# Kernel optimization log

Hardware: AMD Instinct MI355X
Metric: run time of the kernel (lower is better)

The kernel has to match this reference:

```python
import jax, jax.numpy as jnp
import numpy as np

DIM = 256
NUM_HEADS = 4
HEAD_DIM = DIM // NUM_HEADS


def _linear_params(k, d_in, d_out):
    kw, kb = jax.random.split(k)
    lim = 1.0 / np.sqrt(d_in)
    W = jax.random.uniform(kw, (d_out, d_in), jnp.float32, -lim, lim)
    b = jax.random.uniform(kb, (d_out,), jnp.float32, -lim, lim)
    return W, b


def setup_inputs() -> dict:
    key = jax.random.key(0)
    ks = jax.random.split(key, 10)
    B, Nq, Nkv = 8, 4096, 256
    inp = {
        'node_emb': jax.random.normal(ks[0], (B, Nq, DIM), jnp.float32),
        'cluster_emb': jax.random.normal(ks[1], (B, Nkv, DIM), jnp.float32),
        'clustering_weights': jax.random.normal(ks[2], (B, Nq, Nkv), jnp.float32),
        'ln_q_g': jnp.ones((DIM,), jnp.float32), 'ln_q_b': jnp.zeros((DIM,), jnp.float32),
        'ln_kv_g': jnp.ones((DIM,), jnp.float32), 'ln_kv_b': jnp.zeros((DIM,), jnp.float32),
        'ln_out_g': jnp.ones((DIM,), jnp.float32), 'ln_out_b': jnp.zeros((DIM,), jnp.float32),
    }
    for name, k in [('q', ks[3]), ('k', ks[4]), ('v', ks[5]), ('o', ks[6])]:
        W, b = _linear_params(k, DIM, DIM)
        inp[f'W_{name}'], inp[f'b_{name}'] = W, b
    W1, b1 = _linear_params(ks[7], DIM, DIM)
    W2, b2 = _linear_params(ks[8], DIM, DIM)
    inp.update(W_m1=W1, b_m1=b1, W_m2=W2, b_m2=b2)
    return inp


def _layer_norm(x, g, b, eps=1e-5):
    mu = jnp.mean(x, axis=-1, keepdims=True)
    var = jnp.var(x, axis=-1, keepdims=True)
    return (x - mu) * jax.lax.rsqrt(var + eps) * g + b


def reference(node_emb, cluster_emb, clustering_weights,
              ln_q_g, ln_q_b, ln_kv_g, ln_kv_b, ln_out_g, ln_out_b,
              W_q, b_q, W_k, b_k, W_v, b_v, W_o, b_o,
              W_m1, b_m1, W_m2, b_m2):
    B, Nq, D = node_emb.shape
    Nkv = cluster_emb.shape[1]
    q_in = _layer_norm(node_emb, ln_q_g, ln_q_b)
    kv_in = _layer_norm(cluster_emb, ln_kv_g, ln_kv_b)
    # projections -> [B, H, N, hd]
    Q = (q_in @ W_q.T + b_q).reshape(B, Nq, NUM_HEADS, HEAD_DIM).transpose(0, 2, 1, 3)
    K = (kv_in @ W_k.T + b_k).reshape(B, Nkv, NUM_HEADS, HEAD_DIM).transpose(0, 2, 1, 3)
    V = (kv_in @ W_v.T + b_v).reshape(B, Nkv, NUM_HEADS, HEAD_DIM).transpose(0, 2, 1, 3)
    scores = jnp.einsum('bhqd,bhkd->bhqk', Q, K) / np.sqrt(HEAD_DIM)
    scores = scores + clustering_weights[:, None, :, :]
    attn = jax.nn.softmax(scores, axis=-1)
    ctx = jnp.einsum('bhqk,bhkd->bhqd', attn, V)
    ctx = ctx.transpose(0, 2, 1, 3).reshape(B, Nq, D)
    attn_out = ctx @ W_o.T + b_o
    x = node_emb + attn_out
    h = _layer_norm(x, ln_out_g, ln_out_b)
    h = jax.nn.gelu(h @ W_m1.T + b_m1, approximate=False) @ W_m2.T + b_m2
    out = x + h
    attn_matrix = attn.mean(axis=1)
    return out, attn_matrix
```

## Files before the change

kernel.cpp:

```cpp
#include <hip/hip_runtime.h>
#include <math.h>

typedef __attribute__((ext_vector_type(8))) short short8;
typedef __attribute__((ext_vector_type(4))) float f32x4;
typedef __attribute__((ext_vector_type(2))) unsigned int u32x2;

#define AS1 __attribute__((address_space(1)))
#define AS3 __attribute__((address_space(3)))

__device__ __forceinline__ float b2f(short s){
  return __uint_as_float(((unsigned int)(unsigned short)s) << 16);
}
__device__ __forceinline__ short f2b(float f){
  unsigned int u = __float_as_uint(f);
  u = (u + 0x7fffu + ((u >> 16) & 1u)) >> 16;
  return (short)u;
}
__device__ __forceinline__ unsigned pk2(float lo, float hi){
  return ((unsigned)(unsigned short)f2b(hi) << 16) | (unsigned)(unsigned short)f2b(lo);
}
__device__ __forceinline__ float ulo(unsigned u){ return __uint_as_float(u << 16); }
__device__ __forceinline__ float uhi(unsigned u){ return __uint_as_float(u & 0xffff0000u); }

__global__ __launch_bounds__(256) void cvt_w(
    const float* __restrict__ s0, const float* __restrict__ s1,
    const float* __restrict__ s2, const float* __restrict__ s3,
    const float* __restrict__ s4, const float* __restrict__ s5,
    short* __restrict__ dst, short* __restrict__ dstS)
{
  const float* srcs[6] = {s0, s1, s2, s3, s4, s5};
  int i = blockIdx.x * 256 + threadIdx.x;
  int mat = i >> 16, rc = i & 65535;
  short v = f2b(srcs[mat][rc]);
  dst[i] = v;
  int slot = (mat >= 3) ? (mat - 3) : (mat == 0 ? 3 : -1);
  if (slot >= 0){
    int row = rc >> 8, col = rc & 255;
    int d2 = slot * 65536 + ((col >> 5) << 13) + (row << 5)
           + (((col >> 3) & 3) << 3) + (col & 7);
    dstS[d2] = v;
  }
}

__global__ __launch_bounds__(256, 2) void kv_k(
    const float* __restrict__ cluster,
    const short* __restrict__ Wk, const short* __restrict__ Wv,
    const float* __restrict__ b_k, const float* __restrict__ b_v,
    const float* __restrict__ lng, const float* __restrict__ lnb,
    short* __restrict__ kfrag, short* __restrict__ vfrag)
{
  __shared__ short As[64][264];
  __shared__ short Ws[2][256][40];
  const int tid = threadIdx.x;
  const int m0 = blockIdx.x << 6;
  const int w = tid >> 6, lane = tid & 63;
  const int l15 = lane & 15, g = lane >> 4;

  {
    const int row = tid >> 2, c0 = (tid & 3) << 6;
    float vv[64];
    const float* src = &cluster[(size_t)(m0 + row) * 256 + c0];
    #pragma unroll
    for (int i = 0; i < 16; ++i) *(f32x4*)&vv[4 * i] = *(const f32x4*)&src[4 * i];
    float s1 = 0.f, s2 = 0.f;
    #pragma unroll
    for (int i = 0; i < 64; ++i){ s1 += vv[i]; s2 += vv[i] * vv[i]; }
    s1 += __shfl_xor(s1, 1); s2 += __shfl_xor(s2, 1);
    s1 += __shfl_xor(s1, 2); s2 += __shfl_xor(s2, 2);
    const float mu = s1 * 0.00390625f;
    const float rs = rsqrtf(s2 * 0.00390625f - mu * mu + 1e-5f);
    #pragma unroll
    for (int i = 0; i < 8; ++i){
      f32x4 gv0 = *(const f32x4*)&lng[c0 + 8 * i];
      f32x4 gv1 = *(const f32x4*)&lng[c0 + 8 * i + 4];
      f32x4 bv0 = *(const f32x4*)&lnb[c0 + 8 * i];
      f32x4 bv1 = *(const f32x4*)&lnb[c0 + 8 * i + 4];
      short8 o;
      #pragma unroll
      for (int j = 0; j < 4; ++j) o[j] = f2b((vv[8 * i + j] - mu) * rs * gv0[j] + bv0[j]);
      #pragma unroll
      for (int j = 0; j < 4; ++j) o[4 + j] = f2b((vv[8 * i + 4 + j] - mu) * rs * gv1[j] + bv1[j]);
      *(short8*)&As[row][c0 + 8 * i] = o;
    }
  }

  f32x4 acc[16];
  const int row_l = (w << 4) + (g << 2);

#define KV_LOOP(WMAT)                                                                 \
  do{                                                                                 \
    _Pragma("unroll")                                                                 \
    for (int it = 0; it < 4; ++it){                                                   \
      int row = (it << 6) + (tid >> 2), c = (tid & 3) << 3;                           \
      *(short8*)&Ws[0][row][c] = *(const short8*)&(WMAT)[(size_t)row * 256 + c];      \
    }                                                                                 \
    __syncthreads();                                                                  \
    _Pragma("unroll")                                                                 \
    for (int nt = 0; nt < 16; ++nt) acc[nt] = (f32x4){0.f, 0.f, 0.f, 0.f};            \
    int cur = 0;                                                                      \
    for (int s = 0; s < 8; ++s){                                                      \
      const int k0 = s << 5;                                                          \
      short8 wreg[4];                                                                 \
      if (s < 7){                                                                     \
        _Pragma("unroll")                                                             \
        for (int it = 0; it < 4; ++it)                                                \
          wreg[it] = *(const short8*)&(WMAT)[(size_t)((it << 6) + (tid >> 2)) * 256 + k0 + 32 + ((tid & 3) << 3)]; \
      }                                                                               \
      short8 af = *(const short8*)&As[(w << 4) + l15][k0 + (g << 3)];                 \
      _Pragma("unroll")                                                               \
      for (int nt = 0; nt < 16; ++nt){                                                \
        short8 bf = *(const short8*)&Ws[cur][(nt << 4) + l15][g << 3];                \
        acc[nt] = __builtin_amdgcn_mfma_f32_16x16x32_bf16(af, bf, acc[nt], 0, 0, 0);  \
      }                                                                               \
      if (s < 7){                                                                     \
        _Pragma("unroll")                                                             \
        for (int it = 0; it < 4; ++it)                                                \
          *(short8*)&Ws[cur ^ 1][(it << 6) + (tid >> 2)][(tid & 3) << 3] = wreg[it];  \
      }                                                                               \
      __syncthreads();                                                                \
      cur ^= 1;                                                                       \
    }                                                                                 \
  }while(0)

  KV_LOOP(Wk);
  #pragma unroll
  for (int nt = 0; nt < 16; ++nt){
    const int col = (nt << 4) + l15;
    const float bv = b_k[col];
    #pragma unroll
    for (int r = 0; r < 4; ++r){
      const int m = m0 + row_l + r;
      float v = acc[nt][r] + bv;
      const int b_ = m >> 8, kvr = m & 255;
      const int knt = kvr >> 4, kl = kvr & 15;
      const int h = col >> 6, half = (col >> 5) & 1, kg = (col >> 3) & 3, kj = col & 7;
      kfrag[(((((size_t)(b_ * 4 + h) * 16 + knt) * 2 + half) * 4 + kg) * 16 + kl) * 8 + kj] = f2b(v);
    }
  }
  KV_LOOP(Wv);
  #pragma unroll
  for (int nt = 0; nt < 16; ++nt){
    const int col = (nt << 4) + l15;
    const float bv = b_v[col];
    #pragma unroll
    for (int r = 0; r < 4; ++r){
      const int m = m0 + row_l + r;
      float v = acc[nt][r] + bv;
      const int b_ = m >> 8, kvj = m & 255;
      const int jp = (kvj & ~31) | (((kvj >> 2) & 3) << 3) | (((kvj >> 4) & 1) << 2) | (kvj & 3);
      const int h = col >> 6, dp = col & 63;
      const int kk = jp >> 5, vg = (jp >> 3) & 3, vj = jp & 7;
      const int vn2 = dp >> 4, vl = dp & 15;
      vfrag[(((((size_t)(b_ * 4 + h) * 8 + kk) * 4 + vn2) * 4 + vg) * 16 + vl) * 8 + vj] = f2b(v);
    }
  }
#undef KV_LOOP
}

__global__ __launch_bounds__(512, 4) void qgemm_k(
    const float* __restrict__ node, const short* __restrict__ Wq,
    const float* __restrict__ bias,
    const float* __restrict__ lng, const float* __restrict__ lnb,
    short* __restrict__ outB)
{
  extern __shared__ __align__(16) short lds[];
  short* Ws0 = lds + 16896;
  short* Ws1 = Ws0 + 8192;
  const int tid = threadIdx.x;
  const int tile = blockIdx.x;
  const int m0 = tile << 6;
  const int w = tid >> 6, lane = tid & 63;
  const int l15 = lane & 15, g = lane >> 4;
  const int wm = w >> 1, wn = w & 1;
  const int row_l = (wm << 4) + (g << 2);
  const int colb = wn << 7;

#define ASW8(row_, col0_) (*(short8*)((char*)lds + (row_) * 528 + \
    (((col0_) << 1) ^ ((((row_) >> 2) & 3) << 4))))
#define ASR8(row_, boff_) (*(const short8*)((char*)lds + (row_) * 528 + \
    ((boff_) ^ ((((row_) >> 2) & 3) << 4))))
#define STGW(dst_, wmat_, s_) do{ _Pragma("unroll")                                  \
  for (int it_ = 0; it_ < 2; ++it_){ int c_ = (it_ << 9) + tid;                      \
    __builtin_amdgcn_global_load_lds(                                               \
        (const AS1 void*)((wmat_) + ((size_t)(s_) << 13) + (c_ << 3)),              \
        (AS3 void*)((dst_) + (c_ << 3)), 16, 0, 0); } }while(0)

  {
    const int row = tid >> 3, c0 = (tid & 7) << 5;
    float vv[32];
    const float* src = &node[(size_t)(m0 + row) * 256 + c0];
    #pragma unroll
    for (int i = 0; i < 8; ++i) *(f32x4*)&vv[4 * i] = *(const f32x4*)&src[4 * i];
    float s1 = 0.f, s2 = 0.f;
    #pragma unroll
    for (int i = 0; i < 32; ++i){ s1 += vv[i]; s2 += vv[i] * vv[i]; }
    s1 += __shfl_xor(s1, 1); s2 += __shfl_xor(s2, 1);
    s1 += __shfl_xor(s1, 2); s2 += __shfl_xor(s2, 2);
    s1 += __shfl_xor(s1, 4); s2 += __shfl_xor(s2, 4);
    const float mu = s1 * 0.00390625f;
    const float rs = rsqrtf(s2 * 0.00390625f - mu * mu + 1e-5f);
    #pragma unroll
    for (int i = 0; i < 4; ++i){
      const int col0 = c0 + 8 * i;
      f32x4 g0 = *(const f32x4*)&lng[col0], g1 = *(const f32x4*)&lng[col0 + 4];
      f32x4 b0 = *(const f32x4*)&lnb[col0], b1 = *(const f32x4*)&lnb[col0 + 4];
      short8 o;
      #pragma unroll
      for (int j = 0; j < 4; ++j) o[j] = f2b((vv[8 * i + j] - mu) * rs * g0[j] + b0[j]);
      #pragma unroll
      for (int j = 0; j < 4; ++j) o[4 + j] = f2b((vv[8 * i + 4 + j] - mu) * rs * g1[j] + b1[j]);
      ASW8(row, col0) = o;
    }
  }
  STGW(Ws0, Wq, 0);
  __syncthreads();

  f32x4 acc[8];
  #pragma unroll
  for (int ntl = 0; ntl < 8; ++ntl) acc[ntl] = {0.f, 0.f, 0.f, 0.f};
  {
    int cur = 0;
    #pragma unroll
    for (int s = 0; s < 8; ++s){
      short* rbuf = cur ? Ws1 : Ws0;
      short* sbuf = cur ? Ws0 : Ws1;
      if (s < 7){ STGW(sbuf, Wq, s + 1);
        asm volatile("s_waitcnt vmcnt(2)" ::: "memory");
      } else {
        asm volatile("s_waitcnt vmcnt(0)" ::: "memory");
      }
      __builtin_amdgcn_s_barrier();
      __builtin_amdgcn_sched_barrier(0);
      const short8 af = ASR8((wm << 4) + l15, (s << 6) + (g << 4));
      __builtin_amdgcn_s_setprio(1);
      #pragma unroll
      for (int ntl = 0; ntl < 8; ++ntl){
        short8 bf = *(const short8*)&rbuf[(((wn << 3) + ntl) * 16 + l15) * 32 + (g << 3)];
        acc[ntl] = __builtin_amdgcn_mfma_f32_16x16x32_bf16(af, bf, acc[ntl], 0, 0, 0);
      }
      __builtin_amdgcn_s_setprio(0);
      __builtin_amdgcn_s_barrier();
      __builtin_amdgcn_sched_barrier(0);
      cur ^= 1;
    }
  }
  #pragma unroll
  for (int ntl = 0; ntl < 8; ++ntl){
    const int col = colb + (ntl << 4) + l15;
    const float bv = bias[col];
    #pragma unroll
    for (int r = 0; r < 4; ++r){
      float v = acc[ntl][r] + bv;
      outB[((((size_t)tile * 8 + (col >> 5)) * 4 + wm) * 64
            + (((col >> 3) & 3) << 4) + (g << 2) + r) * 8 + (col & 7)] = f2b(v);
    }
  }
#undef ASW8
#undef ASR8
#undef STGW
}

__global__ __launch_bounds__(256, 2) void attn_k(
    const short* __restrict__ Qf, const short* __restrict__ Kf,
    const short* __restrict__ Vf, const float* __restrict__ cw,
    short* __restrict__ ctx, float* __restrict__ am_out)
{
  extern __shared__ __align__(16) short smem[];
  short* Kl = smem;
  short* Vl = smem + 16384;
  const int b = blockIdx.y;
  const int q0 = blockIdx.x << 6;
  const int tid = threadIdx.x;
  const int w = tid >> 6, lane = tid & 63;
  const int l15 = lane & 15, g = lane >> 4;
  const size_t qw = (size_t)b * 4096 + q0 + (w << 4);
  const size_t qblk = qw >> 4;
  const size_t tileQ = qblk >> 2;
  const int wQ = (int)(qblk & 3);
  const size_t tileC = (size_t)b * 64 + blockIdx.x;

#define STG(dst_, src_) do{ _Pragma("unroll")                                        \
  for (int it_ = 0; it_ < 8; ++it_){ int c_ = (it_ << 8) + tid;                      \
    __builtin_amdgcn_global_load_lds((const AS1 void*)((src_) + (c_ << 3)),          \
                                     (AS3 void*)((dst_) + (c_ << 3)), 16, 0, 0); } }while(0)

  STG(Kl, Kf + ((size_t)(b * 4) << 14));

  unsigned cwp[16][2];
  f32x4 am[16];
  {
    char* reg = (char*)smem + 32768 + (w << 13);
    #pragma unroll
    for (int j = 0; j < 16; ++j){
      f32x4 v = *(const f32x4*)&cw[(qw + j) * 256 + (lane << 2)];
      u32x2 d = { pk2(v[0], v[1]), pk2(v[2], v[3]) };
      unsigned off = ((j << 9) + (lane << 3)) ^ ((j & 7) << 4);
      *(u32x2*)(reg + off) = d;
    }
    __syncthreads();
    #pragma unroll
    for (int nt = 0; nt < 16; ++nt){
      unsigned base = ((l15 << 9) + (nt << 5) + (g << 3)) ^ ((l15 & 7) << 4);
      cwp[nt][0] = *(const unsigned*)(reg + base);
      cwp[nt][1] = *(const unsigned*)(reg + base + 4);
      am[nt] = {0.f, 0.f, 0.f, 0.f};
    }
    __syncthreads();
  }

  for (int h = 0; h < 4; ++h){
    STG(Vl, Vf + ((size_t)(b * 4 + h) << 14));
    short8 qf0 = *(const short8*)&Qf[(((tileQ * 8 + (h << 1)) * 4 + wQ) * 64 + lane) * 8];
    short8 qf1 = *(const short8*)&Qf[(((tileQ * 8 + (h << 1) + 1) * 4 + wQ) * 64 + lane) * 8];

    f32x4 acc[16];
    #pragma unroll
    for (int nt = 0; nt < 16; ++nt) acc[nt] = {0.f, 0.f, 0.f, 0.f};
    __builtin_amdgcn_s_setprio(1);
    #pragma unroll
    for (int nt = 0; nt < 16; ++nt){
      short8 kf0 = *(const short8*)&Kl[(nt << 10) + (lane << 3)];
      acc[nt] = __builtin_amdgcn_mfma_f32_16x16x32_bf16(kf0, qf0, acc[nt], 0, 0, 0);
      short8 kf1 = *(const short8*)&Kl[(nt << 10) + 512 + (lane << 3)];
      acc[nt] = __builtin_amdgcn_mfma_f32_16x16x32_bf16(kf1, qf1, acc[nt], 0, 0, 0);
    }
    __builtin_amdgcn_s_setprio(0);
    __syncthreads();
    if (h < 3) STG(Kl, Kf + ((size_t)(b * 4 + h + 1) << 14));

    float mx = -3.4e38f;
    #pragma unroll
    for (int nt = 0; nt < 16; ++nt){
      float c0 = __uint_as_float(cwp[nt][0] << 16);
      float c1 = __uint_as_float(cwp[nt][0] & 0xffff0000u);
      float c2 = __uint_as_float(cwp[nt][1] << 16);
      float c3 = __uint_as_float(cwp[nt][1] & 0xffff0000u);
      acc[nt][0] = acc[nt][0] * 0.125f + c0;
      acc[nt][1] = acc[nt][1] * 0.125f + c1;
      acc[nt][2] = acc[nt][2] * 0.125f + c2;
      acc[nt][3] = acc[nt][3] * 0.125f + c3;
      mx = fmaxf(mx, fmaxf(fmaxf(acc[nt][0], acc[nt][1]), fmaxf(acc[nt][2], acc[nt][3])));
    }
    mx = fmaxf(mx, __shfl_xor(mx, 16));
    mx = fmaxf(mx, __shfl_xor(mx, 32));
    float sm = 0.f;
    #pragma unroll
    for (int nt = 0; nt < 16; ++nt){
      #pragma unroll
      for (int r = 0; r < 4; ++r){
        float e = __expf(acc[nt][r] - mx);
        acc[nt][r] = e; sm += e;
      }
    }
    sm += __shfl_xor(sm, 16);
    sm += __shfl_xor(sm, 32);
    float inv = 1.f / sm;
    #pragma unroll
    for (int nt = 0; nt < 16; ++nt){
      #pragma unroll
      for (int r = 0; r < 4; ++r){
        float p = acc[nt][r] * inv;
        acc[nt][r] = p;
        am[nt][r] += 0.25f * p;
      }
    }
    f32x4 oc[4] = {{0,0,0,0},{0,0,0,0},{0,0,0,0},{0,0,0,0}};
    __builtin_amdgcn_s_setprio(1);
    #pragma unroll
    for (int kk = 0; kk < 8; ++kk){
      union { short8 s; unsigned u[4]; } pa;
      pa.u[0] = pk2(acc[2 * kk][0],     acc[2 * kk][1]);
      pa.u[1] = pk2(acc[2 * kk][2],     acc[2 * kk][3]);
      pa.u[2] = pk2(acc[2 * kk + 1][0], acc[2 * kk + 1][1]);
      pa.u[3] = pk2(acc[2 * kk + 1][2], acc[2 * kk + 1][3]);
      #pragma unroll
      for (int n2 = 0; n2 < 4; ++n2){
        short8 vb = *(const short8*)&Vl[(((kk << 2) + n2) << 9) + (lane << 3)];
        oc[n2] = __builtin_amdgcn_mfma_f32_16x16x32_bf16(pa.s, vb, oc[n2], 0, 0, 0);
      }
    }
    __builtin_amdgcn_s_setprio(0);
    #pragma unroll
    for (int n2 = 0; n2 < 4; ++n2){
      const int sctx = (h << 1) + (n2 >> 1);
      const int gctx = ((n2 & 1) << 1) + (l15 >> 3);
      const int j = l15 & 7;
      #pragma unroll
      for (int r = 0; r < 4; ++r)
        ctx[(((tileC * 8 + sctx) * 4 + w) * 64 + (gctx << 4) + (g << 2) + r) * 8 + j]
            = f2b(oc[n2][r]);
    }
    __syncthreads();
  }

  {
    char* reg = (char*)smem + (w << 14);
    #pragma unroll
    for (int nt = 0; nt < 16; ++nt){
      unsigned off = ((l15 << 10) + (nt << 6) + (g << 4)) ^ ((l15 & 7) << 4);
      *(f32x4*)(reg + off) = am[nt];
    }
    __syncthreads();
    #pragma unroll
    for (int i2 = 0; i2 < 16; ++i2){
      unsigned fb = (tid << 4) + (i2 << 12);
      unsigned rowin = (fb >> 10) & 15;
      f32x4 v = *(const f32x4*)((char*)smem + (fb ^ ((rowin & 7) << 4)));
      unsigned row = fb >> 10;
      *(f32x4*)&am_out[((size_t)b * 4096 + q0 + row) * 256 + ((fb & 1023) >> 2)] = v;
    }
  }
#undef STG
}

__global__ __launch_bounds__(512, 4) void tail_k(
    const short* __restrict__ ctxaf, const short* __restrict__ Wst,
    const float* __restrict__ b_o, const float* __restrict__ b_m1,
    const float* __restrict__ b_m2, const float* __restrict__ node,
    const float* __restrict__ lng, const float* __restrict__ lnb,
    float* __restrict__ outF)
{
  extern __shared__ __align__(16) short lds[];
  short* Ws0 = lds + 16896;
  short* Ws1 = Ws0 + 8192;
  float* part = (float*)(lds + 33280);
  const int tid = threadIdx.x;
  const int tile = blockIdx.x;
  const int m0 = tile << 6;
  const int w = tid >> 6, lane = tid & 63;
  const int l15 = lane & 15, g = lane >> 4;
  const int wm = w >> 1, wn = w & 1;
  const int row_l = (wm << 4) + (g << 2);
  const int colb = wn << 7;

#define ASW(row_, col_) (*(short*)((char*)lds + (row_) * 528 + \
    (((col_) ^ ((((row_) >> 2) & 3) << 3)) << 1)))
#define ASR8(row_, boff_) (*(const short8*)((char*)lds + (row_) * 528 + \
    ((boff_) ^ ((((row_) >> 2) & 3) << 4))))
#define STGW(dst_, wmat_, s_) do{ _Pragma("unroll")                                  \
  for (int it_ = 0; it_ < 2; ++it_){ int c_ = (it_ << 9) + tid;                      \
    __builtin_amdgcn_global_load_lds(                                               \
        (const AS1 void*)((wmat_) + ((size_t)(s_) << 13) + (c_ << 3)),              \
        (AS3 void*)((dst_) + (c_ << 3)), 16, 0, 0); } }while(0)
#define KLOOP(WMAT, AF_EXPR)                                                         \
  do{ int cur = 0;                                                                   \
    _Pragma("unroll")                                                                \
    for (int s = 0; s < 8; ++s){                                                     \
      short* rbuf = cur ? Ws1 : Ws0;                                                 \
      short* sbuf = cur ? Ws0 : Ws1;                                                 \
      if (s < 7){ STGW(sbuf, WMAT, s + 1);                                           \
        asm volatile("s_waitcnt vmcnt(2)" ::: "memory");                             \
      } else {                                                                       \
        asm volatile("s_waitcnt vmcnt(0)" ::: "memory");                             \
      }                                                                              \
      __builtin_amdgcn_s_barrier();                                                  \
      __builtin_amdgcn_sched_barrier(0);                                             \
      const short8 af = (AF_EXPR);                                                   \
      __builtin_amdgcn_s_setprio(1);                                                 \
      _Pragma("unroll")                                                              \
      for (int ntl = 0; ntl < 8; ++ntl){                                             \
        short8 bf = *(const short8*)&rbuf[(((wn << 3) + ntl) * 16 + l15) * 32 + (g << 3)]; \
        acc[ntl] = __builtin_amdgcn_mfma_f32_16x16x32_bf16(af, bf, acc[ntl], 0, 0, 0); \
      }                                                                              \
      __builtin_amdgcn_s_setprio(0);                                                 \
      __builtin_amdgcn_s_barrier();                                                  \
      __builtin_amdgcn_sched_barrier(0);                                             \
      cur ^= 1;                                                                      \
    } }while(0)

  f32x4 acc[8];

  STGW(Ws0, Wst, 0);
  short8 afr[8];
  #pragma unroll
  for (int s = 0; s < 8; ++s)
    afr[s] = *(const short8*)&ctxaf[((((size_t)tile << 3) + s) * 4 + wm) * 512 + (lane << 3)];
  #pragma unroll
  for (int ntl = 0; ntl < 8; ++ntl) acc[ntl] = {0.f, 0.f, 0.f, 0.f};
  KLOOP(Wst, afr[s]);

  unsigned xvp[8][2];
  #pragma unroll
  for (int ntl = 0; ntl < 8; ++ntl){
    const int col = colb + (ntl << 4) + l15;
    const float bv = b_o[col];
    float x0 = acc[ntl][0] + bv + node[(size_t)(m0 + row_l + 0) * 256 + col];
    float x1 = acc[ntl][1] + bv + node[(size_t)(m0 + row_l + 1) * 256 + col];
    float x2 = acc[ntl][2] + bv + node[(size_t)(m0 + row_l + 2) * 256 + col];
    float x3 = acc[ntl][3] + bv + node[(size_t)(m0 + row_l + 3) * 256 + col];
    xvp[ntl][0] = pk2(x0, x1);
    xvp[ntl][1] = pk2(x2, x3);
  }
  #pragma unroll
  for (int r = 0; r < 4; ++r){
    float s1 = 0.f, s2 = 0.f;
    #pragma unroll
    for (int ntl = 0; ntl < 8; ++ntl){
      float v = (r == 0) ? ulo(xvp[ntl][0]) : (r == 1) ? uhi(xvp[ntl][0])
              : (r == 2) ? ulo(xvp[ntl][1]) : uhi(xvp[ntl][1]);
      s1 += v; s2 += v * v;
    }
    #pragma unroll
    for (int off = 1; off < 16; off <<= 1){ s1 += __shfl_xor(s1, off); s2 += __shfl_xor(s2, off); }
    if (l15 == 0){
      part[((row_l + r) * 2 + wn) * 2]     = s1;
      part[((row_l + r) * 2 + wn) * 2 + 1] = s2;
    }
  }
  __syncthreads();
  #pragma unroll
  for (int r = 0; r < 4; ++r){
    const int row = row_l + r;
    const float S1 = part[(row * 2) * 2]     + part[(row * 2 + 1) * 2];
    const float S2 = part[(row * 2) * 2 + 1] + part[(row * 2 + 1) * 2 + 1];
    const float mu = S1 * 0.00390625f;
    const float rs = rsqrtf(S2 * 0.00390625f - mu * mu + 1e-5f);
    #pragma unroll
    for (int ntl = 0; ntl < 8; ++ntl){
      const int col = colb + (ntl << 4) + l15;
      float v = (r == 0) ? ulo(xvp[ntl][0]) : (r == 1) ? uhi(xvp[ntl][0])
              : (r == 2) ? ulo(xvp[ntl][1]) : uhi(xvp[ntl][1]);
      ASW(row, col) = f2b((v - mu) * rs * lng[col] + lnb[col]);
    }
  }

  {
    const short* Wm1 = Wst + 65536;
    STGW(Ws0, Wm1, 0);
    __syncthreads();
    #pragma unroll
    for (int ntl = 0; ntl < 8; ++ntl) acc[ntl] = {0.f, 0.f, 0.f, 0.f};
    KLOOP(Wm1, ASR8((wm << 4) + l15, (s << 6) + (g << 4)));
  }
  #pragma unroll
  for (int ntl = 0; ntl < 8; ++ntl){
    const int col = colb + (ntl << 4) + l15;
    const float bv = b_m1[col];
    #pragma unroll
    for (int r = 0; r < 4; ++r){
      float v = acc[ntl][r] + bv;
      v = 0.5f * v * (1.0f + erff(v * 0.70710678118f));
      ASW(row_l + r, col) = f2b(v);
    }
  }

  {
    const short* Wm2 = Wst + 131072;
    STGW(Ws0, Wm2, 0);
    __syncthreads();
    #pragma unroll
    for (int ntl = 0; ntl < 8; ++ntl) acc[ntl] = {0.f, 0.f, 0.f, 0.f};
    KLOOP(Wm2, ASR8((wm << 4) + l15, (s << 6) + (g << 4)));
  }
  #pragma unroll
  for (int ntl = 0; ntl < 8; ++ntl){
    const int col = colb + (ntl << 4) + l15;
    const float bv = b_m2[col];
    #pragma unroll
    for (int r = 0; r < 4; ++r){
      float xr = (r == 0) ? ulo(xvp[ntl][0]) : (r == 1) ? uhi(xvp[ntl][0])
               : (r == 2) ? ulo(xvp[ntl][1]) : uhi(xvp[ntl][1]);
      outF[(size_t)(m0 + row_l + r) * 256 + col] = acc[ntl][r] + bv + xr;
    }
  }
#undef ASW
#undef ASR8
#undef STGW
#undef KLOOP
}

extern "C" void kernel_launch(void* const* d_in, const int* in_sizes, int n_in,
                              void* d_out, int out_size, void* d_ws, size_t ws_size,
                              hipStream_t stream)
{
  const float* node_emb = (const float*)d_in[0];
  const float* cluster  = (const float*)d_in[1];
  const float* cw       = (const float*)d_in[2];
  const float* ln_q_g   = (const float*)d_in[3];
  const float* ln_q_b   = (const float*)d_in[4];
  const float* ln_kv_g  = (const float*)d_in[5];
  const float* ln_kv_b  = (const float*)d_in[6];
  const float* ln_o_g   = (const float*)d_in[7];
  const float* ln_o_b   = (const float*)d_in[8];
  const float* W_q  = (const float*)d_in[9];  const float* b_q  = (const float*)d_in[10];
  const float* W_k  = (const float*)d_in[11]; const float* b_k  = (const float*)d_in[12];
  const float* W_v  = (const float*)d_in[13]; const float* b_v  = (const float*)d_in[14];
  const float* W_o  = (const float*)d_in[15]; const float* b_o  = (const float*)d_in[16];
  const float* W_m1 = (const float*)d_in[17]; const float* b_m1 = (const float*)d_in[18];
  const float* W_m2 = (const float*)d_in[19]; const float* b_m2 = (const float*)d_in[20];

  char* ws = (char*)d_ws;
  short* Wbf   = (short*)ws;
  short* Wst   = (short*)(ws + 786432);
  short* bufA  = (short*)(ws + 1310720);
  short* bufB  = (short*)(ws + 1310720 + 16777216);
  short* kfrag = (short*)(ws + 1310720 + 2 * 16777216);
  short* vfrag = (short*)(ws + 1310720 + 2 * 16777216 + 1048576);

  float* outF = (float*)d_out;
  float* amof = (float*)d_out + 8388608;

  hipFuncSetAttribute((const void*)attn_k,  hipFuncAttributeMaxDynamicSharedMemorySize, 65536);
  hipFuncSetAttribute((const void*)tail_k,  hipFuncAttributeMaxDynamicSharedMemorySize, 67584);
  hipFuncSetAttribute((const void*)qgemm_k, hipFuncAttributeMaxDynamicSharedMemorySize, 66560);

  cvt_w<<<1536, 256, 0, stream>>>(W_q, W_k, W_v, W_o, W_m1, W_m2, Wbf, Wst);
  kv_k<<<32, 256, 0, stream>>>(cluster, Wbf + 65536, Wbf + 131072,
      b_k, b_v, ln_kv_g, ln_kv_b, kfrag, vfrag);
  qgemm_k<<<512, 512, 66560, stream>>>(node_emb, Wst + 196608, b_q,
      ln_q_g, ln_q_b, bufB);
  attn_k<<<dim3(64, 8), 256, 65536, stream>>>(bufB, kfrag, vfrag, cw, bufA, amof);
  tail_k<<<512, 512, 67584, stream>>>(bufA, Wst, b_o, b_m1, b_m2,
      node_emb, ln_o_g, ln_o_b, outF);
}
```

Baseline: 115.5 us.

## Split attention key dimension across two waves per query block

The attention kernel now runs 512 threads per block, and pairs of waves split the 256 keys for each 16-query group. Row max and row sum are combined through small LDS buffers behind extra barriers, and the partial P·V outputs are added through LDS before the context is written. The goal is to halve per-wave register pressure (accumulators, clustering weights, attention-mean state) and raise the number of resident waves so latency is hidden better. In exchange it adds several block-wide barriers per head and extra LDS traffic for the reductions.

```diff
diff --git a/kernel.cpp b/kernel.cpp
--- a/kernel.cpp
+++ b/kernel.cpp
@@ -172,7 +172,6 @@
   const int w = tid >> 6, lane = tid & 63;
   const int l15 = lane & 15, g = lane >> 4;
   const int wm = w >> 1, wn = w & 1;
-  const int row_l = (wm << 4) + (g << 2);
   const int colb = wn << 7;
 
 #define ASW8(row_, col0_) (*(short8*)((char*)lds + (row_) * 528 + \
@@ -260,7 +259,7 @@
 #undef STGW
 }
 
-__global__ __launch_bounds__(256, 2) void attn_k(
+__global__ __launch_bounds__(512, 4) void attn_k(
     const short* __restrict__ Qf, const short* __restrict__ Kf,
     const short* __restrict__ Vf, const float* __restrict__ cw,
     short* __restrict__ ctx, float* __restrict__ am_out)
@@ -268,39 +267,47 @@
   extern __shared__ __align__(16) short smem[];
   short* Kl = smem;
   short* Vl = smem + 16384;
+  float* mb = (float*)((char*)smem + 65536);
+  float* sb = mb + 128;
   const int b = blockIdx.y;
   const int q0 = blockIdx.x << 6;
   const int tid = threadIdx.x;
   const int w = tid >> 6, lane = tid & 63;
   const int l15 = lane & 15, g = lane >> 4;
-  const size_t qw = (size_t)b * 4096 + q0 + (w << 4);
+  const int wq = w >> 1, wk = w & 1;
+  const int arow = (wq << 4) + l15;
+  const size_t qw = (size_t)b * 4096 + q0 + (wq << 4);
   const size_t qblk = qw >> 4;
   const size_t tileQ = qblk >> 2;
   const int wQ = (int)(qblk & 3);
   const size_t tileC = (size_t)b * 64 + blockIdx.x;
 
 #define STG(dst_, src_) do{ _Pragma("unroll")                                        \
-  for (int it_ = 0; it_ < 8; ++it_){ int c_ = (it_ << 8) + tid;                      \
+  for (int it_ = 0; it_ < 4; ++it_){ int c_ = (it_ << 9) + tid;                      \
     __builtin_amdgcn_global_load_lds((const AS1 void*)((src_) + (c_ << 3)),          \
                                      (AS3 void*)((dst_) + (c_ << 3)), 16, 0, 0); } }while(0)
+#define LBAR() do{ asm volatile("s_waitcnt lgkmcnt(0)" ::: "memory");                \
+  __builtin_amdgcn_s_barrier(); __builtin_amdgcn_sched_barrier(0); }while(0)
 
   STG(Kl, Kf + ((size_t)(b * 4) << 14));
 
-  unsigned cwp[16][2];
-  f32x4 am[16];
+  unsigned cwp[8][2];
+  f32x4 am[8];
   {
-    char* reg = (char*)smem + 32768 + (w << 13);
-    #pragma unroll
-    for (int j = 0; j < 16; ++j){
-      f32x4 v = *(const f32x4*)&cw[(qw + j) * 256 + (lane << 2)];
+    char* reg = (char*)Vl;
+    #pragma unroll
+    for (int jj = 0; jj < 8; ++jj){
+      const int row = (w << 3) + jj;
+      f32x4 v = *(const f32x4*)&cw[((size_t)b * 4096 + q0 + row) * 256 + (lane << 2)];
       u32x2 d = { pk2(v[0], v[1]), pk2(v[2], v[3]) };
-      unsigned off = ((j << 9) + (lane << 3)) ^ ((j & 7) << 4);
+      unsigned off = ((unsigned)(row << 9) + (lane << 3)) ^ ((row & 7) << 4);
       *(u32x2*)(reg + off) = d;
     }
     __syncthreads();
     #pragma unroll
-    for (int nt = 0; nt < 16; ++nt){
-      unsigned base = ((l15 << 9) + (nt << 5) + (g << 3)) ^ ((l15 & 7) << 4);
+    for (int nt = 0; nt < 8; ++nt){
+      const int ntp = (wk << 3) + nt;
+      unsigned base = ((unsigned)(arow << 9) + (ntp << 5) + (g << 3)) ^ ((arow & 7) << 4);
       cwp[nt][0] = *(const unsigned*)(reg + base);
       cwp[nt][1] = *(const unsigned*)(reg + base + 4);
       am[nt] = {0.f, 0.f, 0.f, 0.f};
@@ -313,15 +320,16 @@
     short8 qf0 = *(const short8*)&Qf[(((tileQ * 8 + (h << 1)) * 4 + wQ) * 64 + lane) * 8];
     short8 qf1 = *(const short8*)&Qf[(((tileQ * 8 + (h << 1) + 1) * 4 + wQ) * 64 + lane) * 8];
 
-    f32x4 acc[16];
-    #pragma unroll
-    for (int nt = 0; nt < 16; ++nt) acc[nt] = {0.f, 0.f, 0.f, 0.f};
+    f32x4 acc[8];
+    #pragma unroll
+    for (int nt = 0; nt < 8; ++nt) acc[nt] = {0.f, 0.f, 0.f, 0.f};
     __builtin_amdgcn_s_setprio(1);
     #pragma unroll
-    for (int nt = 0; nt < 16; ++nt){
-      short8 kf0 = *(const short8*)&Kl[(nt << 10) + (lane << 3)];
+    for (int nt = 0; nt < 8; ++nt){
+      const int ntp = (wk << 3) + nt;
+      short8 kf0 = *(const short8*)&Kl[(ntp << 10) + (lane << 3)];
       acc[nt] = __builtin_amdgcn_mfma_f32_16x16x32_bf16(kf0, qf0, acc[nt], 0, 0, 0);
-      short8 kf1 = *(const short8*)&Kl[(nt << 10) + 512 + (lane << 3)];
+      short8 kf1 = *(const short8*)&Kl[(ntp << 10) + 512 + (lane << 3)];
       acc[nt] = __builtin_amdgcn_mfma_f32_16x16x32_bf16(kf1, qf1, acc[nt], 0, 0, 0);
     }
     __builtin_amdgcn_s_setprio(0);
@@ -330,11 +338,9 @@
 
     float mx = -3.4e38f;
     #pragma unroll
-    for (int nt = 0; nt < 16; ++nt){
-      float c0 = __uint_as_float(cwp[nt][0] << 16);
-      float c1 = __uint_as_float(cwp[nt][0] & 0xffff0000u);
-      float c2 = __uint_as_float(cwp[nt][1] << 16);
-      float c3 = __uint_as_float(cwp[nt][1] & 0xffff0000u);
+    for (int nt = 0; nt < 8; ++nt){
+      float c0 = ulo(cwp[nt][0]), c1 = uhi(cwp[nt][0]);
+      float c2 = ulo(cwp[nt][1]), c3 = uhi(cwp[nt][1]);
       acc[nt][0] = acc[nt][0] * 0.125f + c0;
       acc[nt][1] = acc[nt][1] * 0.125f + c1;
       acc[nt][2] = acc[nt][2] * 0.125f + c2;
@@ -343,20 +349,25 @@
     }
     mx = fmaxf(mx, __shfl_xor(mx, 16));
     mx = fmaxf(mx, __shfl_xor(mx, 32));
+    if (g == 0) mb[arow * 2 + wk] = mx;
+    LBAR();
+    const float m = fmaxf(mb[arow * 2], mb[arow * 2 + 1]);
     float sm = 0.f;
     #pragma unroll
-    for (int nt = 0; nt < 16; ++nt){
+    for (int nt = 0; nt < 8; ++nt){
       #pragma unroll
       for (int r = 0; r < 4; ++r){
-        float e = __expf(acc[nt][r] - mx);
+        float e = __expf(acc[nt][r] - m);
         acc[nt][r] = e; sm += e;
       }
     }
     sm += __shfl_xor(sm, 16);
     sm += __shfl_xor(sm, 32);
-    float inv = 1.f / sm;
-    #pragma unroll
-    for (int nt = 0; nt < 16; ++nt){
+    if (g == 0) sb[arow * 2 + wk] = sm;
+    LBAR();
+    const float inv = 1.f / (sb[arow * 2] + sb[arow * 2 + 1]);
+    #pragma unroll
+    for (int nt = 0; nt < 8; ++nt){
       #pragma unroll
       for (int r = 0; r < 4; ++r){
         float p = acc[nt][r] * inv;
@@ -367,50 +378,62 @@
     f32x4 oc[4] = {{0,0,0,0},{0,0,0,0},{0,0,0,0},{0,0,0,0}};
     __builtin_amdgcn_s_setprio(1);
     #pragma unroll
-    for (int kk = 0; kk < 8; ++kk){
+    for (int kkl = 0; kkl < 4; ++kkl){
+      const int kkg = (wk << 2) + kkl;
       union { short8 s; unsigned u[4]; } pa;
-      pa.u[0] = pk2(acc[2 * kk][0],     acc[2 * kk][1]);
-      pa.u[1] = pk2(acc[2 * kk][2],     acc[2 * kk][3]);
-      pa.u[2] = pk2(acc[2 * kk + 1][0], acc[2 * kk + 1][1]);
-      pa.u[3] = pk2(acc[2 * kk + 1][2], acc[2 * kk + 1][3]);
+      pa.u[0] = pk2(acc[2 * kkl][0],     acc[2 * kkl][1]);
+      pa.u[1] = pk2(acc[2 * kkl][2],     acc[2 * kkl][3]);
+      pa.u[2] = pk2(acc[2 * kkl + 1][0], acc[2 * kkl + 1][1]);
+      pa.u[3] = pk2(acc[2 * kkl + 1][2], acc[2 * kkl + 1][3]);
       #pragma unroll
       for (int n2 = 0; n2 < 4; ++n2){
-        short8 vb = *(const short8*)&Vl[(((kk << 2) + n2) << 9) + (lane << 3)];
+        short8 vb = *(const short8*)&Vl[(((kkg << 2) + n2) << 9) + (lane << 3)];
         oc[n2] = __builtin_amdgcn_mfma_f32_16x16x32_bf16(pa.s, vb, oc[n2], 0, 0, 0);
       }
     }
     __builtin_amdgcn_s_setprio(0);
-    #pragma unroll
-    for (int n2 = 0; n2 < 4; ++n2){
-      const int sctx = (h << 1) + (n2 >> 1);
-      const int gctx = ((n2 & 1) << 1) + (l15 >> 3);
-      const int j = l15 & 7;
-      #pragma unroll
-      for (int r = 0; r < 4; ++r)
-        ctx[(((tileC * 8 + sctx) * 4 + w) * 64 + (gctx << 4) + (g << 2) + r) * 8 + j]
-            = f2b(oc[n2][r]);
+    LBAR();
+    float* obuf = (float*)Vl;
+    if (wk == 0){
+      #pragma unroll
+      for (int n2 = 0; n2 < 4; ++n2)
+        *(f32x4*)&obuf[wq * 1024 + n2 * 256 + lane * 4] = oc[n2];
+    }
+    LBAR();
+    if (wk == 1){
+      #pragma unroll
+      for (int n2 = 0; n2 < 4; ++n2){
+        f32x4 t = *(const f32x4*)&obuf[wq * 1024 + n2 * 256 + lane * 4];
+        const int sctx = (h << 1) + (n2 >> 1);
+        const int gctx = ((n2 & 1) << 1) + (l15 >> 3);
+        const int j = l15 & 7;
+        #pragma unroll
+        for (int r = 0; r < 4; ++r)
+          ctx[(((tileC * 8 + sctx) * 4 + wq) * 64 + (gctx << 4) + (g << 2) + r) * 8 + j]
+              = f2b(oc[n2][r] + t[r]);
+      }
     }
     __syncthreads();
   }
 
   {
-    char* reg = (char*)smem + (w << 14);
-    #pragma unroll
-    for (int nt = 0; nt < 16; ++nt){
-      unsigned off = ((l15 << 10) + (nt << 6) + (g << 4)) ^ ((l15 & 7) << 4);
-      *(f32x4*)(reg + off) = am[nt];
-    }
-    __syncthreads();
-    #pragma unroll
-    for (int i2 = 0; i2 < 16; ++i2){
-      unsigned fb = (tid << 4) + (i2 << 12);
-      unsigned rowin = (fb >> 10) & 15;
-      f32x4 v = *(const f32x4*)((char*)smem + (fb ^ ((rowin & 7) << 4)));
+    #pragma unroll
+    for (int nt = 0; nt < 8; ++nt){
+      unsigned off = ((unsigned)(wq << 14) + (l15 << 10) + (wk << 9) + (nt << 6) + (g << 4))
+                   ^ ((l15 & 7) << 4);
+      *(f32x4*)((char*)smem + off) = am[nt];
+    }
+    LBAR();
+    #pragma unroll
+    for (int i2 = 0; i2 < 8; ++i2){
+      unsigned fb = (tid << 4) + (i2 << 13);
       unsigned row = fb >> 10;
+      f32x4 v = *(const f32x4*)((char*)smem + (fb ^ ((row & 7) << 4)));
       *(f32x4*)&am_out[((size_t)b * 4096 + q0 + row) * 256 + ((fb & 1023) >> 2)] = v;
     }
   }
 #undef STG
+#undef LBAR
 }
 
 __global__ __launch_bounds__(512, 4) void tail_k(
@@ -600,7 +623,7 @@
   float* outF = (float*)d_out;
   float* amof = (float*)d_out + 8388608;
 
-  hipFuncSetAttribute((const void*)attn_k,  hipFuncAttributeMaxDynamicSharedMemorySize, 65536);
+  hipFuncSetAttribute((const void*)attn_k,  hipFuncAttributeMaxDynamicSharedMemorySize, 66560);
   hipFuncSetAttribute((const void*)tail_k,  hipFuncAttributeMaxDynamicSharedMemorySize, 67584);
   hipFuncSetAttribute((const void*)qgemm_k, hipFuncAttributeMaxDynamicSharedMemorySize, 66560);
 
@@ -609,7 +632,7 @@
       b_k, b_v, ln_kv_g, ln_kv_b, kfrag, vfrag);
   qgemm_k<<<512, 512, 66560, stream>>>(node_emb, Wst + 196608, b_q,
       ln_q_g, ln_q_b, bufB);
-  attn_k<<<dim3(64, 8), 256, 65536, stream>>>(bufB, kfrag, vfrag, cw, bufA, amof);
+  attn_k<<<dim3(64, 8), 512, 66560, stream>>>(bufB, kfrag, vfrag, cw, bufA, amof);
   tail_k<<<512, 512, 67584, stream>>>(bufA, Wst, b_o, b_m1, b_m2,
       node_emb, ln_o_g, ln_o_b, outF);
 }
```

After: 133.4 us. 1.16x slower.

## Merge KV projection into Q GEMM kernel and drop plain bf16 weight copy

Applied to the files above, without the earlier changes.

Removes the separate kv_k kernel and folds the K/V projections into the Q projection kernel. The first 32 blocks of the combined launch handle cluster rows, doing K then V with the same pipelined LDS GEMM loop, and the remaining 512 blocks handle node rows. The weight conversion kernel now writes only the swizzled layout for all six matrices, dropping the row-major bf16 copy. This saves one kernel launch and the small, poorly parallel kv_k pass. The trade-off is that the 32 KV blocks each run two GEMMs and may finish after the Q blocks, leaving a short tail.

```diff
diff --git a/kernel.cpp b/kernel.cpp
--- a/kernel.cpp
+++ b/kernel.cpp
@@ -26,154 +26,40 @@
     const float* __restrict__ s0, const float* __restrict__ s1,
     const float* __restrict__ s2, const float* __restrict__ s3,
     const float* __restrict__ s4, const float* __restrict__ s5,
-    short* __restrict__ dst, short* __restrict__ dstS)
+    short* __restrict__ dstS)
 {
   const float* srcs[6] = {s0, s1, s2, s3, s4, s5};
   int i = blockIdx.x * 256 + threadIdx.x;
   int mat = i >> 16, rc = i & 65535;
   short v = f2b(srcs[mat][rc]);
-  dst[i] = v;
-  int slot = (mat >= 3) ? (mat - 3) : (mat == 0 ? 3 : -1);
-  if (slot >= 0){
-    int row = rc >> 8, col = rc & 255;
-    int d2 = slot * 65536 + ((col >> 5) << 13) + (row << 5)
-           + (((col >> 3) & 3) << 3) + (col & 7);
-    dstS[d2] = v;
-  }
-}
-
-__global__ __launch_bounds__(256, 2) void kv_k(
-    const float* __restrict__ cluster,
-    const short* __restrict__ Wk, const short* __restrict__ Wv,
-    const float* __restrict__ b_k, const float* __restrict__ b_v,
-    const float* __restrict__ lng, const float* __restrict__ lnb,
-    short* __restrict__ kfrag, short* __restrict__ vfrag)
-{
-  __shared__ short As[64][264];
-  __shared__ short Ws[2][256][40];
-  const int tid = threadIdx.x;
-  const int m0 = blockIdx.x << 6;
-  const int w = tid >> 6, lane = tid & 63;
-  const int l15 = lane & 15, g = lane >> 4;
-
-  {
-    const int row = tid >> 2, c0 = (tid & 3) << 6;
-    float vv[64];
-    const float* src = &cluster[(size_t)(m0 + row) * 256 + c0];
-    #pragma unroll
-    for (int i = 0; i < 16; ++i) *(f32x4*)&vv[4 * i] = *(const f32x4*)&src[4 * i];
-    float s1 = 0.f, s2 = 0.f;
-    #pragma unroll
-    for (int i = 0; i < 64; ++i){ s1 += vv[i]; s2 += vv[i] * vv[i]; }
-    s1 += __shfl_xor(s1, 1); s2 += __shfl_xor(s2, 1);
-    s1 += __shfl_xor(s1, 2); s2 += __shfl_xor(s2, 2);
-    const float mu = s1 * 0.00390625f;
-    const float rs = rsqrtf(s2 * 0.00390625f - mu * mu + 1e-5f);
-    #pragma unroll
-    for (int i = 0; i < 8; ++i){
-      f32x4 gv0 = *(const f32x4*)&lng[c0 + 8 * i];
-      f32x4 gv1 = *(const f32x4*)&lng[c0 + 8 * i + 4];
-      f32x4 bv0 = *(const f32x4*)&lnb[c0 + 8 * i];
-      f32x4 bv1 = *(const f32x4*)&lnb[c0 + 8 * i + 4];
-      short8 o;
-      #pragma unroll
-      for (int j = 0; j < 4; ++j) o[j] = f2b((vv[8 * i + j] - mu) * rs * gv0[j] + bv0[j]);
-      #pragma unroll
-      for (int j = 0; j < 4; ++j) o[4 + j] = f2b((vv[8 * i + 4 + j] - mu) * rs * gv1[j] + bv1[j]);
-      *(short8*)&As[row][c0 + 8 * i] = o;
-    }
-  }
-
-  f32x4 acc[16];
-  const int row_l = (w << 4) + (g << 2);
-
-#define KV_LOOP(WMAT)                                                                 \
-  do{                                                                                 \
-    _Pragma("unroll")                                                                 \
-    for (int it = 0; it < 4; ++it){                                                   \
-      int row = (it << 6) + (tid >> 2), c = (tid & 3) << 3;                           \
-      *(short8*)&Ws[0][row][c] = *(const short8*)&(WMAT)[(size_t)row * 256 + c];      \
-    }                                                                                 \
-    __syncthreads();                                                                  \
-    _Pragma("unroll")                                                                 \
-    for (int nt = 0; nt < 16; ++nt) acc[nt] = (f32x4){0.f, 0.f, 0.f, 0.f};            \
-    int cur = 0;                                                                      \
-    for (int s = 0; s < 8; ++s){                                                      \
-      const int k0 = s << 5;                                                          \
-      short8 wreg[4];                                                                 \
-      if (s < 7){                                                                     \
-        _Pragma("unroll")                                                             \
-        for (int it = 0; it < 4; ++it)                                                \
-          wreg[it] = *(const short8*)&(WMAT)[(size_t)((it << 6) + (tid >> 2)) * 256 + k0 + 32 + ((tid & 3) << 3)]; \
-      }                                                                               \
-      short8 af = *(const short8*)&As[(w << 4) + l15][k0 + (g << 3)];                 \
-      _Pragma("unroll")                                                               \
-      for (int nt = 0; nt < 16; ++nt){                                                \
-        short8 bf = *(const short8*)&Ws[cur][(nt << 4) + l15][g << 3];                \
-        acc[nt] = __builtin_amdgcn_mfma_f32_16x16x32_bf16(af, bf, acc[nt], 0, 0, 0);  \
-      }                                                                               \
-      if (s < 7){                                                                     \
-        _Pragma("unroll")                                                             \
-        for (int it = 0; it < 4; ++it)                                                \
-          *(short8*)&Ws[cur ^ 1][(it << 6) + (tid >> 2)][(tid & 3) << 3] = wreg[it];  \
-      }                                                                               \
-      __syncthreads();                                                                \
-      cur ^= 1;                                                                       \
-    }                                                                                 \
-  }while(0)
-
-  KV_LOOP(Wk);
-  #pragma unroll
-  for (int nt = 0; nt < 16; ++nt){
-    const int col = (nt << 4) + l15;
-    const float bv = b_k[col];
-    #pragma unroll
-    for (int r = 0; r < 4; ++r){
-      const int m = m0 + row_l + r;
-      float v = acc[nt][r] + bv;
-      const int b_ = m >> 8, kvr = m & 255;
-      const int knt = kvr >> 4, kl = kvr & 15;
-      const int h = col >> 6, half = (col >> 5) & 1, kg = (col >> 3) & 3, kj = col & 7;
-      kfrag[(((((size_t)(b_ * 4 + h) * 16 + knt) * 2 + half) * 4 + kg) * 16 + kl) * 8 + kj] = f2b(v);
-    }
-  }
-  KV_LOOP(Wv);
-  #pragma unroll
-  for (int nt = 0; nt < 16; ++nt){
-    const int col = (nt << 4) + l15;
-    const float bv = b_v[col];
-    #pragma unroll
-    for (int r = 0; r < 4; ++r){
-      const int m = m0 + row_l + r;
-      float v = acc[nt][r] + bv;
-      const int b_ = m >> 8, kvj = m & 255;
-      const int jp = (kvj & ~31) | (((kvj >> 2) & 3) << 3) | (((kvj >> 4) & 1) << 2) | (kvj & 3);
-      const int h = col >> 6, dp = col & 63;
-      const int kk = jp >> 5, vg = (jp >> 3) & 3, vj = jp & 7;
-      const int vn2 = dp >> 4, vl = dp & 15;
-      vfrag[(((((size_t)(b_ * 4 + h) * 8 + kk) * 4 + vn2) * 4 + vg) * 16 + vl) * 8 + vj] = f2b(v);
-    }
-  }
-#undef KV_LOOP
-}
-
-__global__ __launch_bounds__(512, 4) void qgemm_k(
-    const float* __restrict__ node, const short* __restrict__ Wq,
-    const float* __restrict__ bias,
-    const float* __restrict__ lng, const float* __restrict__ lnb,
-    short* __restrict__ outB)
+  int slot = (mat + 3) % 6;
+  int row = rc >> 8, col = rc & 255;
+  int d2 = slot * 65536 + ((col >> 5) << 13) + (row << 5)
+         + (((col >> 3) & 3) << 3) + (col & 7);
+  dstS[d2] = v;
+}
+
+__global__ __launch_bounds__(512, 4) void qkv_k(
+    const float* __restrict__ node, const float* __restrict__ cluster,
+    const short* __restrict__ Wst,
+    const float* __restrict__ b_q, const float* __restrict__ b_k,
+    const float* __restrict__ b_v,
+    const float* __restrict__ lnqg, const float* __restrict__ lnqb,
+    const float* __restrict__ lnkg, const float* __restrict__ lnkb,
+    short* __restrict__ qaf, short* __restrict__ kfrag, short* __restrict__ vfrag)
 {
   extern __shared__ __align__(16) short lds[];
   short* Ws0 = lds + 16896;
   short* Ws1 = Ws0 + 8192;
   const int tid = threadIdx.x;
-  const int tile = blockIdx.x;
-  const int m0 = tile << 6;
   const int w = tid >> 6, lane = tid & 63;
   const int l15 = lane & 15, g = lane >> 4;
   const int wm = w >> 1, wn = w & 1;
   const int row_l = (wm << 4) + (g << 2);
   const int colb = wn << 7;
+  const int isKV = (blockIdx.x < 32);
+  const int tile = isKV ? blockIdx.x : (blockIdx.x - 32);
+  const int m0 = tile << 6;
 
 #define ASW8(row_, col0_) (*(short8*)((char*)lds + (row_) * 528 + \
     (((col0_) << 1) ^ ((((row_) >> 2) & 3) << 4))))
@@ -184,11 +70,39 @@
     __builtin_amdgcn_global_load_lds(                                               \
         (const AS1 void*)((wmat_) + ((size_t)(s_) << 13) + (c_ << 3)),              \
         (AS3 void*)((dst_) + (c_ << 3)), 16, 0, 0); } }while(0)
+#define KLOOP(WMAT)                                                                  \
+  do{ int cur = 0;                                                                   \
+    _Pragma("unroll")                                                                \
+    for (int s = 0; s < 8; ++s){                                                     \
+      short* rbuf = cur ? Ws1 : Ws0;                                                 \
+      short* sbuf = cur ? Ws0 : Ws1;                                                 \
+      if (s < 7){ STGW(sbuf, WMAT, s + 1);                                           \
+        asm volatile("s_waitcnt vmcnt(2)" ::: "memory");                             \
+      } else {                                                                       \
+        asm volatile("s_waitcnt vmcnt(0)" ::: "memory");                             \
+      }                                                                              \
+      __builtin_amdgcn_s_barrier();                                                  \
+      __builtin_amdgcn_sched_barrier(0);                                             \
+      const short8 af = ASR8((wm << 4) + l15, (s << 6) + (g << 4));                  \
+      __builtin_amdgcn_s_setprio(1);                                                 \
+      _Pragma("unroll")                                                              \
+      for (int ntl = 0; ntl < 8; ++ntl){                                             \
+        short8 bf = *(const short8*)&rbuf[(((wn << 3) + ntl) * 16 + l15) * 32 + (g << 3)]; \
+        acc[ntl] = __builtin_amdgcn_mfma_f32_16x16x32_bf16(af, bf, acc[ntl], 0, 0, 0); \
+      }                                                                              \
+      __builtin_amdgcn_s_setprio(0);                                                 \
+      __builtin_amdgcn_s_barrier();                                                  \
+      __builtin_amdgcn_sched_barrier(0);                                             \
+      cur ^= 1;                                                                      \
+    } }while(0)
 
   {
+    const float* srcb = isKV ? cluster : node;
+    const float* lg = isKV ? lnkg : lnqg;
+    const float* lb = isKV ? lnkb : lnqb;
     const int row = tid >> 3, c0 = (tid & 7) << 5;
     float vv[32];
-    const float* src = &node[(size_t)(m0 + row) * 256 + c0];
+    const float* src = &srcb[(size_t)(m0 + row) * 256 + c0];
     #pragma unroll
     for (int i = 0; i < 8; ++i) *(f32x4*)&vv[4 * i] = *(const f32x4*)&src[4 * i];
     float s1 = 0.f, s2 = 0.f;
@@ -202,8 +116,8 @@
     #pragma unroll
     for (int i = 0; i < 4; ++i){
       const int col0 = c0 + 8 * i;
-      f32x4 g0 = *(const f32x4*)&lng[col0], g1 = *(const f32x4*)&lng[col0 + 4];
-      f32x4 b0 = *(const f32x4*)&lnb[col0], b1 = *(const f32x4*)&lnb[col0 + 4];
+      f32x4 g0 = *(const f32x4*)&lg[col0], g1 = *(const f32x4*)&lg[col0 + 4];
+      f32x4 b0 = *(const f32x4*)&lb[col0], b1 = *(const f32x4*)&lb[col0 + 4];
       short8 o;
       #pragma unroll
       for (int j = 0; j < 4; ++j) o[j] = f2b((vv[8 * i + j] - mu) * rs * g0[j] + b0[j]);
@@ -212,52 +126,75 @@
       ASW8(row, col0) = o;
     }
   }
-  STGW(Ws0, Wq, 0);
-  __syncthreads();
 
   f32x4 acc[8];
-  #pragma unroll
-  for (int ntl = 0; ntl < 8; ++ntl) acc[ntl] = {0.f, 0.f, 0.f, 0.f};
-  {
-    int cur = 0;
-    #pragma unroll
-    for (int s = 0; s < 8; ++s){
-      short* rbuf = cur ? Ws1 : Ws0;
-      short* sbuf = cur ? Ws0 : Ws1;
-      if (s < 7){ STGW(sbuf, Wq, s + 1);
-        asm volatile("s_waitcnt vmcnt(2)" ::: "memory");
-      } else {
-        asm volatile("s_waitcnt vmcnt(0)" ::: "memory");
+
+  if (!isKV){
+    const short* Wq = Wst + 196608;
+    STGW(Ws0, Wq, 0);
+    __syncthreads();
+    #pragma unroll
+    for (int ntl = 0; ntl < 8; ++ntl) acc[ntl] = {0.f, 0.f, 0.f, 0.f};
+    KLOOP(Wq);
+    #pragma unroll
+    for (int ntl = 0; ntl < 8; ++ntl){
+      const int col = colb + (ntl << 4) + l15;
+      const float bv = b_q[col];
+      #pragma unroll
+      for (int r = 0; r < 4; ++r){
+        float v = acc[ntl][r] + bv;
+        qaf[((((size_t)tile * 8 + (col >> 5)) * 4 + wm) * 64
+              + (((col >> 3) & 3) << 4) + (g << 2) + r) * 8 + (col & 7)] = f2b(v);
       }
-      __builtin_amdgcn_s_barrier();
-      __builtin_amdgcn_sched_barrier(0);
-      const short8 af = ASR8((wm << 4) + l15, (s << 6) + (g << 4));
-      __builtin_amdgcn_s_setprio(1);
-      #pragma unroll
-      for (int ntl = 0; ntl < 8; ++ntl){
-        short8 bf = *(const short8*)&rbuf[(((wn << 3) + ntl) * 16 + l15) * 32 + (g << 3)];
-        acc[ntl] = __builtin_amdgcn_mfma_f32_16x16x32_bf16(af, bf, acc[ntl], 0, 0, 0);
+    }
+  } else {
+    const short* Wk = Wst + 262144;
+    const short* Wv = Wst + 327680;
+    STGW(Ws0, Wk, 0);
+    __syncthreads();
+    #pragma unroll
+    for (int ntl = 0; ntl < 8; ++ntl) acc[ntl] = {0.f, 0.f, 0.f, 0.f};
+    KLOOP(Wk);
+    #pragma unroll
+    for (int ntl = 0; ntl < 8; ++ntl){
+      const int col = colb + (ntl << 4) + l15;
+      const float bv = b_k[col];
+      const int h = col >> 6, half = (col >> 5) & 1, kg = (col >> 3) & 3, kj = col & 7;
+      #pragma unroll
+      for (int r = 0; r < 4; ++r){
+        const int m = m0 + row_l + r;
+        float v = acc[ntl][r] + bv;
+        const int b_ = m >> 8, kvr = m & 255;
+        const int knt = kvr >> 4, kl = kvr & 15;
+        kfrag[(((((size_t)(b_ * 4 + h) * 16 + knt) * 2 + half) * 4 + kg) * 16 + kl) * 8 + kj] = f2b(v);
       }
-      __builtin_amdgcn_s_setprio(0);
-      __builtin_amdgcn_s_barrier();
-      __builtin_amdgcn_sched_barrier(0);
-      cur ^= 1;
-    }
-  }
-  #pragma unroll
-  for (int ntl = 0; ntl < 8; ++ntl){
-    const int col = colb + (ntl << 4) + l15;
-    const float bv = bias[col];
-    #pragma unroll
-    for (int r = 0; r < 4; ++r){
-      float v = acc[ntl][r] + bv;
-      outB[((((size_t)tile * 8 + (col >> 5)) * 4 + wm) * 64
-            + (((col >> 3) & 3) << 4) + (g << 2) + r) * 8 + (col & 7)] = f2b(v);
+    }
+    STGW(Ws0, Wv, 0);
+    __syncthreads();
+    #pragma unroll
+    for (int ntl = 0; ntl < 8; ++ntl) acc[ntl] = {0.f, 0.f, 0.f, 0.f};
+    KLOOP(Wv);
+    #pragma unroll
+    for (int ntl = 0; ntl < 8; ++ntl){
+      const int col = colb + (ntl << 4) + l15;
+      const float bv = b_v[col];
+      const int h = col >> 6, dp = col & 63;
+      const int vn2 = dp >> 4, vl = dp & 15;
+      #pragma unroll
+      for (int r = 0; r < 4; ++r){
+        const int m = m0 + row_l + r;
+        float v = acc[ntl][r] + bv;
+        const int b_ = m >> 8, kvj = m & 255;
+        const int jp = (kvj & ~31) | (((kvj >> 2) & 3) << 3) | (((kvj >> 4) & 1) << 2) | (kvj & 3);
+        const int kk = jp >> 5, vg = (jp >> 3) & 3, vj = jp & 7;
+        vfrag[(((((size_t)(b_ * 4 + h) * 8 + kk) * 4 + vn2) * 4 + vg) * 16 + vl) * 8 + vj] = f2b(v);
+      }
     }
   }
 #undef ASW8
 #undef ASR8
 #undef STGW
+#undef KLOOP
 }
 
 __global__ __launch_bounds__(256, 2) void attn_k(
@@ -590,25 +527,22 @@
   const float* W_m2 = (const float*)d_in[19]; const float* b_m2 = (const float*)d_in[20];
 
   char* ws = (char*)d_ws;
-  short* Wbf   = (short*)ws;
-  short* Wst   = (short*)(ws + 786432);
-  short* bufA  = (short*)(ws + 1310720);
-  short* bufB  = (short*)(ws + 1310720 + 16777216);
-  short* kfrag = (short*)(ws + 1310720 + 2 * 16777216);
-  short* vfrag = (short*)(ws + 1310720 + 2 * 16777216 + 1048576);
+  short* Wst   = (short*)ws;
+  short* bufA  = (short*)(ws + 786432);
+  short* bufB  = (short*)(ws + 786432 + 16777216);
+  short* kfrag = (short*)(ws + 786432 + 2 * 16777216);
+  short* vfrag = (short*)(ws + 786432 + 2 * 16777216 + 1048576);
 
   float* outF = (float*)d_out;
   float* amof = (float*)d_out + 8388608;
 
-  hipFuncSetAttribute((const void*)attn_k,  hipFuncAttributeMaxDynamicSharedMemorySize, 65536);
-  hipFuncSetAttribute((const void*)tail_k,  hipFuncAttributeMaxDynamicSharedMemorySize, 67584);
-  hipFuncSetAttribute((const void*)qgemm_k, hipFuncAttributeMaxDynamicSharedMemorySize, 66560);
-
-  cvt_w<<<1536, 256, 0, stream>>>(W_q, W_k, W_v, W_o, W_m1, W_m2, Wbf, Wst);
-  kv_k<<<32, 256, 0, stream>>>(cluster, Wbf + 65536, Wbf + 131072,
-      b_k, b_v, ln_kv_g, ln_kv_b, kfrag, vfrag);
-  qgemm_k<<<512, 512, 66560, stream>>>(node_emb, Wst + 196608, b_q,
-      ln_q_g, ln_q_b, bufB);
+  hipFuncSetAttribute((const void*)attn_k, hipFuncAttributeMaxDynamicSharedMemorySize, 65536);
+  hipFuncSetAttribute((const void*)tail_k, hipFuncAttributeMaxDynamicSharedMemorySize, 67584);
+  hipFuncSetAttribute((const void*)qkv_k,  hipFuncAttributeMaxDynamicSharedMemorySize, 66560);
+
+  cvt_w<<<1536, 256, 0, stream>>>(W_q, W_k, W_v, W_o, W_m1, W_m2, Wst);
+  qkv_k<<<544, 512, 66560, stream>>>(node_emb, cluster, Wst,
+      b_q, b_k, b_v, ln_q_g, ln_q_b, ln_kv_g, ln_kv_b, bufB, kfrag, vfrag);
   attn_k<<<dim3(64, 8), 256, 65536, stream>>>(bufB, kfrag, vfrag, cw, bufA, amof);
   tail_k<<<512, 512, 67584, stream>>>(bufA, Wst, b_o, b_m1, b_m2,
       node_emb, ln_o_g, ln_o_b, outF);
```

Result: faster. 104.5 us (-9.5%).
